# Kernel tuning notes

Hardware: AMD Instinct MI355X
Metric: run time of the kernel (lower is better)

## Reference

```python
import jax, jax.numpy as jnp
import numpy as np

B, N, H = 512, 128, 256      # graphs, nodes per graph, hidden
NH, HD = 8, 32               # heads, head dim
DEG = 8
E = B * N * DEG              # 524288 edges
BN_EPS = 1e-5


def setup_inputs() -> dict:
    key = jax.random.key(0)
    ks = jax.random.split(key, 16)

    def w(k, shape):
        return jax.random.normal(k, shape, dtype=jnp.float32) * 0.02

    # intra-graph random edges: base offset per graph, local src/dst in [0, N)
    base = jnp.repeat(jnp.arange(B, dtype=jnp.int32) * N, N * DEG)
    edge_src = base + jax.random.randint(ks[1], (E,), 0, N, dtype=jnp.int32)
    edge_dst = base + jax.random.randint(ks[2], (E,), 0, N, dtype=jnp.int32)

    return {
        "h": jax.random.normal(ks[0], (B * N, H), dtype=jnp.float32),
        "edge_src": edge_src,
        "edge_dst": edge_dst,
        "gin_w1": w(ks[3], (H, H)), "gin_b1": jnp.zeros((H,), jnp.float32),
        "gin_w2": w(ks[4], (H, H)), "gin_b2": jnp.zeros((H,), jnp.float32),
        "attn_in_w": w(ks[5], (3 * H, H)), "attn_in_b": jnp.zeros((3 * H,), jnp.float32),
        "attn_out_w": w(ks[6], (H, H)), "attn_out_b": jnp.zeros((H,), jnp.float32),
        "bn_local_g": jnp.ones((H,), jnp.float32), "bn_local_b": jnp.zeros((H,), jnp.float32),
        "bn_attn_g": jnp.ones((H,), jnp.float32), "bn_attn_b": jnp.zeros((H,), jnp.float32),
        "bn_out_g": jnp.ones((H,), jnp.float32), "bn_out_b": jnp.zeros((H,), jnp.float32),
        "ffn1_w": w(ks[7], (2 * H, H)), "ffn1_b": jnp.zeros((2 * H,), jnp.float32),
        "ffn2_w": w(ks[8], (H, 2 * H)), "ffn2_b": jnp.zeros((H,), jnp.float32),
    }


def _bn(x, g, b):
    # nn.BatchNorm1d training-mode forward: batch stats over node dim, biased var
    mean = jnp.mean(x, axis=0)
    var = jnp.mean(jnp.square(x - mean), axis=0)
    return g * (x - mean) * jax.lax.rsqrt(var + BN_EPS) + b


def _mha(x, in_w, in_b, out_w, out_b):
    # x: [B, N, H]; uniform graphs -> key_padding_mask is all-valid
    qkv = x @ in_w.T + in_b                           # [B, N, 3H]
    q, k, v = jnp.split(qkv, 3, axis=-1)
    def heads(t):
        return t.reshape(B, N, NH, HD).transpose(0, 2, 1, 3)  # [B, NH, N, HD]
    q, k, v = heads(q), heads(k), heads(v)
    scores = jnp.einsum('bhqd,bhkd->bhqk', q, k) / jnp.sqrt(jnp.float32(HD))
    att = jax.nn.softmax(scores, axis=-1)
    o = jnp.einsum('bhqk,bhkd->bhqd', att, v).transpose(0, 2, 1, 3).reshape(B, N, H)
    return o @ out_w.T + out_b


def reference(h, edge_src, edge_dst,
              gin_w1, gin_b1, gin_w2, gin_b2,
              attn_in_w, attn_in_b, attn_out_w, attn_out_b,
              bn_local_g, bn_local_b, bn_attn_g, bn_attn_b, bn_out_g, bn_out_b,
              ffn1_w, ffn1_b, ffn2_w, ffn2_b):
    # --- local GIN branch: (1+eps)*h + sum_{j in N(i)} h_j, eps=0, then 2-layer MLP
    agg = jax.ops.segment_sum(h[edge_src], edge_dst, num_segments=B * N)
    z = h + agg
    h_local = jax.nn.relu(z @ gin_w1.T + gin_b1) @ gin_w2.T + gin_b2
    h_local = _bn(h + h_local, bn_local_g, bn_local_b)

    # --- global attention branch (to_dense_batch is an exact reshape here)
    h_dense = h.reshape(B, N, H)
    h_attn = _mha(h_dense, attn_in_w, attn_in_b, attn_out_w, attn_out_b).reshape(B * N, H)
    h_attn = _bn(h + h_attn, bn_attn_g, bn_attn_b)

    # --- combine + FFN + out norm
    x = h_local + h_attn
    x = x + jax.nn.relu(x @ ffn1_w.T + ffn1_b) @ ffn2_w.T + ffn2_b
    return _bn(x, bn_out_g, bn_out_b)
```

## Files before the change

### kernel.cpp

```cpp
#include <hip/hip_runtime.h>
#include <hip/hip_bf16.h>

#define B_   512
#define N_   128
#define H_   256
#define NH_  8
#define HD_  32
#define DEG_ 8
#define R_   (B_ * N_)
#define E_   (B_ * N_ * DEG_)
#define EPG_ (N_ * DEG_)

typedef unsigned short u16;
typedef unsigned int u32;

typedef __attribute__((ext_vector_type(8))) short s16x8;
typedef __attribute__((ext_vector_type(4))) float f32x4;

__device__ __forceinline__ float b2f(u16 u) {
  union { u32 i; float f; } v;
  v.i = ((u32)u) << 16;
  return v.f;
}
__device__ __forceinline__ u16 f2b(float f) {
  union { float f; u32 u; } v;
  v.f = f;
  u32 r = (v.u + 0x7fffu + ((v.u >> 16) & 1u)) >> 16;
  return (u16)r;
}
__device__ __forceinline__ void ld4b(const u16* p, float* o) {
  ushort4 v = *(const ushort4*)p;
  o[0] = b2f(v.x); o[1] = b2f(v.y); o[2] = b2f(v.z); o[3] = b2f(v.w);
}


#define OFF_GW1 0
#define OFF_GB1 65536
#define OFF_GW2 65792
#define OFF_GB2 131328
#define OFF_AIW 131584
#define OFF_AIB 328192
#define OFF_AOW 328960
#define OFF_AOB 394496
#define OFF_F1W 394752
#define OFF_F1B 525824
#define OFF_F2W 526336
#define OFF_F2B 657408
#define W_TOTAL 657664

__global__ void zero_stats(float* __restrict__ st) {
  st[blockIdx.x * 256 + threadIdx.x] = 0.f;
}

__global__ __launch_bounds__(256) void cvt_h(const float* __restrict__ src,
                                             u16* __restrict__ dst) {
  const size_t i = ((size_t)blockIdx.x * 256 + threadIdx.x) * 4;
  const float4 v = *(const float4*)(src + i);
  ushort4 o;
  o.x = f2b(v.x); o.y = f2b(v.y); o.z = f2b(v.z); o.w = f2b(v.w);
  *(ushort4*)(dst + i) = o;
}

__global__ __launch_bounds__(256) void cvt_w(
    const float* s0, const float* s1, const float* s2, const float* s3,
    const float* s4, const float* s5, const float* s6, const float* s7,
    const float* s8, const float* s9, const float* s10, const float* s11,
    u16* __restrict__ dst) {
  const int sizes[12] = {65536, 256, 65536, 256, 196608, 768,
                         65536, 256, 131072, 512, 131072, 256};
  const float* srcs[12] = {s0, s1, s2, s3, s4, s5, s6, s7, s8, s9, s10, s11};
  int gid = (blockIdx.x * 256 + threadIdx.x) * 4;
  if (gid >= W_TOTAL) return;
  int seg = 0, off = gid;
  while (off >= sizes[seg]) { off -= sizes[seg]; seg++; }
  const float4 v = *(const float4*)(srcs[seg] + off);
  ushort4 o;
  o.x = f2b(v.x); o.y = f2b(v.y); o.z = f2b(v.z); o.w = f2b(v.w);
  *(ushort4*)(dst + gid) = o;
}

#define SROWS_ 32

__global__ __launch_bounds__(256) void agg_kernel(
    const u16* __restrict__ h, const int* __restrict__ esrc,
    const int* __restrict__ edst, u16* __restrict__ z) {
  __shared__ int s_src[EPG_];
  __shared__ int s_cnt[SROWS_];
  __shared__ int s_off[SROWS_ + 1];
  __shared__ int s_pos[SROWS_];
  const int g = blockIdx.x;
  const int r0 = blockIdx.y * SROWS_;
  const int t = threadIdx.x;

  if (t < SROWS_) s_cnt[t] = 0;
  __syncthreads();

  const int ebase = g * EPG_;
  int dl[4], sg[4];
#pragma unroll
  for (int i = 0; i < 4; i++) {
    const int e = ebase + t + i * 256;
    sg[i] = esrc[e];
    dl[i] = edst[e] - g * N_ - r0;
    if ((unsigned)dl[i] < SROWS_) atomicAdd(&s_cnt[dl[i]], 1);
  }
  __syncthreads();
  if (t == 0) {
    int acc = 0;
#pragma unroll
    for (int i = 0; i < SROWS_; i++) { s_off[i] = acc; acc += s_cnt[i]; }
    s_off[SROWS_] = acc;
  }
  __syncthreads();
  if (t < SROWS_) s_pos[t] = s_off[t];
  __syncthreads();
#pragma unroll
  for (int i = 0; i < 4; i++) {
    if ((unsigned)dl[i] < SROWS_) {
      const int slot = atomicAdd(&s_pos[dl[i]], 1);
      s_src[slot] = sg[i];
    }
  }
  __syncthreads();

  const int rg = t >> 5;
  const int c0 = (t & 31) * 8;
  for (int ib = 0; ib < SROWS_; ib += 8) {
    const int i = ib + rg;
    const int row = g * N_ + r0 + i;
    float acc[8];
    {
      const s16x8 v = *(const s16x8*)(h + (size_t)row * H_ + c0);
#pragma unroll
      for (int j = 0; j < 8; j++) acc[j] = b2f((u16)v[j]);
    }
    const int e0 = s_off[i], e1 = s_off[i + 1];
    for (int e = e0; e < e1; e++) {
      const int src = s_src[e];
      const s16x8 v = *(const s16x8*)(h + (size_t)src * H_ + c0);
#pragma unroll
      for (int j = 0; j < 8; j++) acc[j] += b2f((u16)v[j]);
    }
    s16x8 o;
#pragma unroll
    for (int j = 0; j < 8; j++) o[j] = (short)f2b(acc[j]);
    *(s16x8*)(z + (size_t)row * H_ + c0) = o;
  }
}

template <int NC, int K, int RELU, int RES, int STATS, int ASPLIT, int CMODE>
__global__ __launch_bounds__(256) void gemm_mfma(
    const u16* A, const u16* A2,
    const u16* __restrict__ W, const u16* __restrict__ bias,
    const u16* res, u16* C0, u16* C1, u16* C2,
    float* __restrict__ gsum, float* __restrict__ gsq) {
  __shared__ u16 As[128 * 64] __attribute__((aligned(16)));
  __shared__ u16 Bs[128 * 64] __attribute__((aligned(16)));

  const int t = threadIdx.x;
  const int wave = t >> 6, lane = t & 63;
  const int wr = wave >> 1, wc = wave & 1;
  const int quad = lane >> 4, ln15 = lane & 15;
  const int row0 = blockIdx.x * 128, col0 = blockIdx.y * 128;

  f32x4 acc[4][4];
#pragma unroll
  for (int i = 0; i < 4; i++)
#pragma unroll
    for (int j = 0; j < 4; j++) acc[i][j] = (f32x4){0.f, 0.f, 0.f, 0.f};

  for (int kt = 0; kt < K; kt += 64) {
    const u16* Ab;
    int kb, astr;
    if (ASPLIT) {
      if (kt < 256) { Ab = A; kb = kt; } else { Ab = A2; kb = kt - 256; }
      astr = 256;
    } else {
      Ab = A; kb = kt; astr = K;
    }
#pragma unroll
    for (int i = 0; i < 4; i++) {
      const int fid = t + i * 256;
      const u16* ga = Ab + (size_t)(row0 + (fid >> 3)) * astr + kb + (fid & 7) * 8;
      __builtin_amdgcn_global_load_lds(
          (const __attribute__((address_space(1))) void*)ga,
          (__attribute__((address_space(3))) void*)(As + fid * 8), 16, 0, 0);
      const u16* gw = W + (size_t)(col0 + (fid >> 3)) * K + kt + (fid & 7) * 8;
      __builtin_amdgcn_global_load_lds(
          (const __attribute__((address_space(1))) void*)gw,
          (__attribute__((address_space(3))) void*)(Bs + fid * 8), 16, 0, 0);
    }
    __syncthreads();
#pragma unroll
    for (int ks = 0; ks < 64; ks += 32) {
      s16x8 af[4], bf[4];
#pragma unroll
      for (int i = 0; i < 4; i++)
        af[i] = *(const s16x8*)(As + (wr * 64 + i * 16 + ln15) * 64 + ks + quad * 8);
#pragma unroll
      for (int j = 0; j < 4; j++)
        bf[j] = *(const s16x8*)(Bs + (wc * 64 + j * 16 + ln15) * 64 + ks + quad * 8);
#pragma unroll
      for (int i = 0; i < 4; i++)
#pragma unroll
        for (int j = 0; j < 4; j++)
          acc[i][j] = __builtin_amdgcn_mfma_f32_16x16x32_bf16(af[i], bf[j], acc[i][j], 0, 0, 0);
    }
    __syncthreads();
  }

  const int cbase = col0 + wc * 64;
  u16* Cb;
  int coff, cstr;
  if (CMODE) {
    const int chunk = col0 >> 8;
    Cb = (chunk == 0) ? C0 : ((chunk == 1) ? C1 : C2);
    coff = (col0 & 255) + wc * 64;
    cstr = 256;
  } else {
    Cb = C0; coff = cbase; cstr = NC;
  }

  float bs[4];
#pragma unroll
  for (int j = 0; j < 4; j++) bs[j] = b2f(bias[cbase + j * 16 + ln15]);

  float ssum[4] = {}, ssq[4] = {};
#pragma unroll
  for (int i = 0; i < 4; i++) {
    const int rbase = row0 + wr * 64 + i * 16 + quad * 4;
#pragma unroll
    for (int reg = 0; reg < 4; reg++) {
      const int row = rbase + reg;
#pragma unroll
      for (int j = 0; j < 4; j++) {
        float val = acc[i][j][reg] + bs[j];
        if (RELU) val = fmaxf(val, 0.f);
        if (RES) val += b2f(res[(size_t)row * 256 + cbase + j * 16 + ln15]);
        Cb[(size_t)row * cstr + coff + j * 16 + ln15] = f2b(val);
        if (STATS) { ssum[j] += val; ssq[j] += val * val; }
      }
    }
  }

  if (STATS) {
#pragma unroll
    for (int j = 0; j < 4; j++) {
      float s = ssum[j];
      s += __shfl_xor(s, 16);
      s += __shfl_xor(s, 32);
      float q = ssq[j];
      q += __shfl_xor(q, 16);
      q += __shfl_xor(q, 32);
      if (lane < 16) {
        atomicAdd(&gsum[cbase + j * 16 + lane], s);
        atomicAdd(&gsq[cbase + j * 16 + lane], q);
      }
    }
  }
}

__global__ __launch_bounds__(256) void attn_mfma(
    const u16* q, const u16* __restrict__ k,
    const u16* __restrict__ v, u16* o) {
  __shared__ u16 lds[21760] __attribute__((aligned(16)));
  u16* Vt = lds;
  u16* Qs = lds + 4352;
  u16* Ks = lds + 4352 + 5120;
  u16* P  = lds + 4352;

  const int g = blockIdx.x >> 3;
  const int hd = blockIdx.x & 7;
  const int t = threadIdx.x;
  const int wave = t >> 6, lane = t & 63;
  const int quad = lane >> 4, ln15 = lane & 15;
  const int strip = wave * 32;
  const float scale = 0.1767766952966369f;

#pragma unroll
  for (int i = 0; i < 4; i++) {
    const int fid = t + i * 256;
    const int row = fid >> 3;
    const int seg = fid & 7;
    const size_t gidx = (size_t)(g * N_ + row) * H_ + hd * HD_ + seg * 4;
    const ushort4 qv = *(const ushort4*)(q + gidx);
    const ushort4 kv = *(const ushort4*)(k + gidx);
    const ushort4 vv = *(const ushort4*)(v + gidx);
    ushort4 qs;
    qs.x = f2b(b2f(qv.x) * scale); qs.y = f2b(b2f(qv.y) * scale);
    qs.z = f2b(b2f(qv.z) * scale); qs.w = f2b(b2f(qv.w) * scale);
    *(ushort4*)(Qs + row * 40 + seg * 4) = qs;
    *(ushort4*)(Ks + row * 40 + seg * 4) = kv;
    Vt[(seg * 4 + 0) * 136 + row] = vv.x;
    Vt[(seg * 4 + 1) * 136 + row] = vv.y;
    Vt[(seg * 4 + 2) * 136 + row] = vv.z;
    Vt[(seg * 4 + 3) * 136 + row] = vv.w;
  }
  __syncthreads();

  s16x8 af[2], bf[8];
#pragma unroll
  for (int mi = 0; mi < 2; mi++)
    af[mi] = *(const s16x8*)(Qs + (strip + mi * 16 + ln15) * 40 + quad * 8);
#pragma unroll
  for (int nj = 0; nj < 8; nj++)
    bf[nj] = *(const s16x8*)(Ks + (nj * 16 + ln15) * 40 + quad * 8);

  f32x4 acc[2][8];
#pragma unroll
  for (int mi = 0; mi < 2; mi++)
#pragma unroll
    for (int nj = 0; nj < 8; nj++)
      acc[mi][nj] = __builtin_amdgcn_mfma_f32_16x16x32_bf16(
          af[mi], bf[nj], (f32x4){0.f, 0.f, 0.f, 0.f}, 0, 0, 0);

  __syncthreads();

#pragma unroll
  for (int mi = 0; mi < 2; mi++) {
#pragma unroll
    for (int reg = 0; reg < 4; reg++) {
      float mx = acc[mi][0][reg];
#pragma unroll
      for (int j = 1; j < 8; j++) mx = fmaxf(mx, acc[mi][j][reg]);
      mx = fmaxf(mx, __shfl_xor(mx, 1));
      mx = fmaxf(mx, __shfl_xor(mx, 2));
      mx = fmaxf(mx, __shfl_xor(mx, 4));
      mx = fmaxf(mx, __shfl_xor(mx, 8));
      float e[8], s = 0.f;
#pragma unroll
      for (int j = 0; j < 8; j++) { e[j] = __expf(acc[mi][j][reg] - mx); s += e[j]; }
      s += __shfl_xor(s, 1);
      s += __shfl_xor(s, 2);
      s += __shfl_xor(s, 4);
      s += __shfl_xor(s, 8);
      const float inv = 1.f / s;
      const int prow = strip + mi * 16 + quad * 4 + reg;
#pragma unroll
      for (int j = 0; j < 8; j++)
        P[prow * 136 + j * 16 + ln15] = f2b(e[j] * inv);
    }
  }
  __syncthreads();

  f32x4 acc2[2][2];
#pragma unroll
  for (int mi = 0; mi < 2; mi++)
#pragma unroll
    for (int nj = 0; nj < 2; nj++) acc2[mi][nj] = (f32x4){0.f, 0.f, 0.f, 0.f};
#pragma unroll
  for (int kt = 0; kt < 4; kt++) {
    s16x8 paf[2], vbf[2];
#pragma unroll
    for (int mi = 0; mi < 2; mi++)
      paf[mi] = *(const s16x8*)(P + (strip + mi * 16 + ln15) * 136 + kt * 32 + quad * 8);
#pragma unroll
    for (int nj = 0; nj < 2; nj++)
      vbf[nj] = *(const s16x8*)(Vt + (nj * 16 + ln15) * 136 + kt * 32 + quad * 8);
#pragma unroll
    for (int mi = 0; mi < 2; mi++)
#pragma unroll
      for (int nj = 0; nj < 2; nj++)
        acc2[mi][nj] = __builtin_amdgcn_mfma_f32_16x16x32_bf16(
            paf[mi], vbf[nj], acc2[mi][nj], 0, 0, 0);
  }

#pragma unroll
  for (int mi = 0; mi < 2; mi++)
#pragma unroll
    for (int nj = 0; nj < 2; nj++)
#pragma unroll
      for (int reg = 0; reg < 4; reg++) {
        const int row = strip + mi * 16 + quad * 4 + reg;
        o[(size_t)(g * N_ + row) * H_ + hd * HD_ + nj * 16 + ln15] =
            f2b(acc2[mi][nj][reg]);
      }
}

__global__ void bn_finalize(const float* __restrict__ sum,
                            const float* __restrict__ sq,
                            const float* __restrict__ g,
                            const float* __restrict__ bb,
                            float* __restrict__ a, float* __restrict__ b) {
  const int c = threadIdx.x;
  const float mean = sum[c] * (1.f / R_);
  const float var = fmaxf(sq[c] * (1.f / R_) - mean * mean, 0.f);
  const float ai = g[c] * rsqrtf(var + 1e-5f);
  a[c] = ai;
  b[c] = bb[c] - mean * ai;
}

__global__ __launch_bounds__(256) void combine_kernel(
    const u16* __restrict__ rl, const u16* __restrict__ ra,
    const float* __restrict__ st, u16* __restrict__ x) {
  const size_t i = (size_t)blockIdx.x * 256 + threadIdx.x;
  const int col = (int)(i & 63) * 4;
  float rl4[4], ra4[4];
  ld4b(rl + i * 4, rl4);
  ld4b(ra + i * 4, ra4);
  const float* al = st + 1536;
  const float* bl = st + 1792;
  const float* aa = st + 2048;
  const float* ba = st + 2304;
  ushort4 o;
  u16* ov = (u16*)&o;
#pragma unroll
  for (int j = 0; j < 4; j++)
    ov[j] = f2b(al[col + j] * rl4[j] + bl[col + j] + aa[col + j] * ra4[j] + ba[col + j]);
  *(ushort4*)(x + i * 4) = o;
}

__global__ __launch_bounds__(256) void final_kernel(
    const u16* __restrict__ y, const float* __restrict__ st,
    float* __restrict__ out) {
  const size_t i = (size_t)blockIdx.x * 256 + threadIdx.x;
  const int col = (int)(i & 63) * 4;
  float y4[4];
  ld4b(y + i * 4, y4);
  const float* ao = st + 2560;
  const float* bo = st + 2816;
  float4 o;
  o.x = ao[col + 0] * y4[0] + bo[col + 0];
  o.y = ao[col + 1] * y4[1] + bo[col + 1];
  o.z = ao[col + 2] * y4[2] + bo[col + 2];
  o.w = ao[col + 3] * y4[3] + bo[col + 3];
  *(float4*)(out + i * 4) = o;
}

extern "C" void kernel_launch(void* const* d_in, const int* in_sizes, int n_in,
                              void* d_out, int out_size, void* d_ws, size_t ws_size,
                              hipStream_t stream) {
  const float* h = (const float*)d_in[0];
  const int* esrc = (const int*)d_in[1];
  const int* edst = (const int*)d_in[2];
  const float* bn_local_g = (const float*)d_in[11];
  const float* bn_local_b = (const float*)d_in[12];
  const float* bn_attn_g = (const float*)d_in[13];
  const float* bn_attn_b = (const float*)d_in[14];
  const float* bn_out_g = (const float*)d_in[15];
  const float* bn_out_b = (const float*)d_in[16];

  const size_t RH = (size_t)R_ * H_;
  float* stats = (float*)d_ws;
  u16* WB = (u16*)((char*)d_ws + 65536);
  u16* Hb = (u16*)((char*)d_ws + 65536 + 2097152);
  u16* S1 = Hb + RH;
  u16* S2 = S1 + RH;
  u16* OD = (u16*)d_out;
  float* outf = (float*)d_out;

  zero_stats<<<12, 256, 0, stream>>>(stats);
  cvt_h<<<(int)(RH / 4 / 256), 256, 0, stream>>>(h, Hb);
  cvt_w<<<(W_TOTAL / 4 + 255) / 256, 256, 0, stream>>>(
      (const float*)d_in[3], (const float*)d_in[4], (const float*)d_in[5],
      (const float*)d_in[6], (const float*)d_in[7], (const float*)d_in[8],
      (const float*)d_in[9], (const float*)d_in[10], (const float*)d_in[17],
      (const float*)d_in[18], (const float*)d_in[19], (const float*)d_in[20], WB);

  gemm_mfma<768, 256, 0, 0, 0, 0, 1><<<dim3(512, 6), 256, 0, stream>>>(
      Hb, nullptr, WB + OFF_AIW, WB + OFF_AIB, nullptr, S1, S2, OD, nullptr, nullptr);
  attn_mfma<<<B_ * NH_, 256, 0, stream>>>(S1, S2, OD, S1);
  gemm_mfma<256, 256, 0, 1, 1, 0, 0><<<dim3(512, 2), 256, 0, stream>>>(
      S1, nullptr, WB + OFF_AOW, WB + OFF_AOB, Hb, S2, nullptr, nullptr,
      stats + 512, stats + 768);
  agg_kernel<<<dim3(B_, 4), 256, 0, stream>>>(Hb, esrc, edst, OD);
  gemm_mfma<256, 256, 1, 0, 0, 0, 0><<<dim3(512, 2), 256, 0, stream>>>(
      OD, nullptr, WB + OFF_GW1, WB + OFF_GB1, nullptr, S1, nullptr, nullptr,
      nullptr, nullptr);
  gemm_mfma<256, 256, 0, 1, 1, 0, 0><<<dim3(512, 2), 256, 0, stream>>>(
      S1, nullptr, WB + OFF_GW2, WB + OFF_GB2, Hb, OD, nullptr, nullptr,
      stats + 0, stats + 256);

  bn_finalize<<<1, 256, 0, stream>>>(stats + 0, stats + 256, bn_local_g,
                                     bn_local_b, stats + 1536, stats + 1792);
  bn_finalize<<<1, 256, 0, stream>>>(stats + 512, stats + 768, bn_attn_g,
                                     bn_attn_b, stats + 2048, stats + 2304);

  combine_kernel<<<(int)(RH / 4 / 256), 256, 0, stream>>>(OD, S2, stats, S1);
  gemm_mfma<512, 256, 1, 0, 0, 0, 1><<<dim3(512, 4), 256, 0, stream>>>(
      S1, nullptr, WB + OFF_F1W, WB + OFF_F1B, nullptr, S2, OD, nullptr,
      nullptr, nullptr);
  gemm_mfma<256, 512, 0, 1, 1, 1, 0><<<dim3(512, 2), 256, 0, stream>>>(
      S2, OD, WB + OFF_F2W, WB + OFF_F2B, S1, S1, nullptr, nullptr,
      stats + 1024, stats + 1280);

  bn_finalize<<<1, 256, 0, stream>>>(stats + 1024, stats + 1280, bn_out_g,
                                     bn_out_b, stats + 2560, stats + 2816);
  final_kernel<<<(int)(RH / 4 / 256), 256, 0, stream>>>(S1, stats, outf);
}
```

Before: 605.5 us.

## Double-buffer GEMM LDS tiles and XOR-swizzle layout to avoid bank conflicts

The MFMA GEMM now keeps two LDS buffers for A and W and issues the next K-tile's global-to-LDS loads before computing on the current tile, waiting with explicit vmcnt counters instead of full syncthreads. The LDS layout is also XOR-swizzled per row so that the 16-byte fragment reads by each wave hit different banks. This targets global-load latency stalls and LDS bank conflicts. In exchange it doubles LDS use (64KB per block), which may lower occupancy, and it relies on hand-placed waitcnt and barriers being correct.

```diff
diff --git a/kernel.cpp b/kernel.cpp
--- a/kernel.cpp
+++ b/kernel.cpp
@@ -154,8 +154,8 @@
     const u16* __restrict__ W, const u16* __restrict__ bias,
     const u16* res, u16* C0, u16* C1, u16* C2,
     float* __restrict__ gsum, float* __restrict__ gsq) {
-  __shared__ u16 As[128 * 64] __attribute__((aligned(16)));
-  __shared__ u16 Bs[128 * 64] __attribute__((aligned(16)));
+  __shared__ u16 As[2][128 * 64] __attribute__((aligned(16)));
+  __shared__ u16 Bs[2][128 * 64] __attribute__((aligned(16)));
 
   const int t = threadIdx.x;
   const int wave = t >> 6, lane = t & 63;
@@ -169,44 +169,63 @@
 #pragma unroll
     for (int j = 0; j < 4; j++) acc[i][j] = (f32x4){0.f, 0.f, 0.f, 0.f};
 
-  for (int kt = 0; kt < K; kt += 64) {
-    const u16* Ab;
-    int kb, astr;
-    if (ASPLIT) {
-      if (kt < 256) { Ab = A; kb = kt; } else { Ab = A2; kb = kt - 256; }
-      astr = 256;
-    } else {
-      Ab = A; kb = kt; astr = K;
-    }
+  auto stage = [&](int b, int kt) {
 #pragma unroll
     for (int i = 0; i < 4; i++) {
       const int fid = t + i * 256;
-      const u16* ga = Ab + (size_t)(row0 + (fid >> 3)) * astr + kb + (fid & 7) * 8;
+      const int row = fid >> 3;
+      const int segp = (fid & 7) ^ (row & 7);
+      const u16* Ab;
+      int kb;
+      if (ASPLIT) {
+        if (kt < 256) { Ab = A; kb = kt; } else { Ab = A2; kb = kt - 256; }
+      } else {
+        Ab = A; kb = kt;
+      }
+      const int astr = ASPLIT ? 256 : K;
+      const u16* ga = Ab + (size_t)(row0 + row) * astr + kb + segp * 8;
       __builtin_amdgcn_global_load_lds(
           (const __attribute__((address_space(1))) void*)ga,
-          (__attribute__((address_space(3))) void*)(As + fid * 8), 16, 0, 0);
-      const u16* gw = W + (size_t)(col0 + (fid >> 3)) * K + kt + (fid & 7) * 8;
+          (__attribute__((address_space(3))) void*)(&As[b][fid * 8]), 16, 0, 0);
+      const u16* gw = W + (size_t)(col0 + row) * K + kt + segp * 8;
       __builtin_amdgcn_global_load_lds(
           (const __attribute__((address_space(1))) void*)gw,
-          (__attribute__((address_space(3))) void*)(Bs + fid * 8), 16, 0, 0);
-    }
-    __syncthreads();
+          (__attribute__((address_space(3))) void*)(&Bs[b][fid * 8]), 16, 0, 0);
+    }
+  };
+
+  stage(0, 0);
+  for (int kt = 0; kt < K; kt += 64) {
+    const int cur = (kt >> 6) & 1;
+    if (kt + 64 < K) {
+      stage(cur ^ 1, kt + 64);
+      asm volatile("s_waitcnt vmcnt(8)" ::: "memory");
+    } else {
+      asm volatile("s_waitcnt vmcnt(0)" ::: "memory");
+    }
+    __builtin_amdgcn_s_barrier();
 #pragma unroll
     for (int ks = 0; ks < 64; ks += 32) {
       s16x8 af[4], bf[4];
 #pragma unroll
-      for (int i = 0; i < 4; i++)
-        af[i] = *(const s16x8*)(As + (wr * 64 + i * 16 + ln15) * 64 + ks + quad * 8);
-#pragma unroll
-      for (int j = 0; j < 4; j++)
-        bf[j] = *(const s16x8*)(Bs + (wc * 64 + j * 16 + ln15) * 64 + ks + quad * 8);
+      for (int i = 0; i < 4; i++) {
+        const int ra = wr * 64 + i * 16 + ln15;
+        af[i] = *(const s16x8*)(
+            &As[cur][ra * 64 + ((((ks >> 3) + quad) ^ (ra & 7)) * 8)]);
+      }
+#pragma unroll
+      for (int j = 0; j < 4; j++) {
+        const int rb = wc * 64 + j * 16 + ln15;
+        bf[j] = *(const s16x8*)(
+            &Bs[cur][rb * 64 + ((((ks >> 3) + quad) ^ (rb & 7)) * 8)]);
+      }
 #pragma unroll
       for (int i = 0; i < 4; i++)
 #pragma unroll
         for (int j = 0; j < 4; j++)
           acc[i][j] = __builtin_amdgcn_mfma_f32_16x16x32_bf16(af[i], bf[j], acc[i][j], 0, 0, 0);
     }
-    __syncthreads();
+    __builtin_amdgcn_s_barrier();
   }
 
   const int cbase = col0 + wc * 64;
```

Result: no change. 608.6 us (+0.5%).
